# Performance work log

Measured on AMD Instinct MI355X. Metric: run time of the kernel, lower is better.

The kernel has to match this reference:

```python
import jax, jax.numpy as jnp
import numpy as np

B, S, D = 4, 4096, 1024
DC = 1024  # d_chunk (defaults to d_model)
NUM_CLASSES = 4


def setup_inputs() -> dict:
    key = jax.random.key(0)
    ks = jax.random.split(key, 8)
    init = lambda k, shape: (jax.random.normal(k, shape, jnp.float32) * 0.02)
    return {
        "h": jax.random.normal(ks[0], (B, S, D), jnp.float32),
        "pseudo_labels": jax.random.randint(ks[1], (B, S), 0, NUM_CLASSES, jnp.int32),
        "Wl": init(ks[2], (D, NUM_CLASSES)), "bl": jnp.zeros((NUM_CLASSES,), jnp.float32),
        "Wq": init(ks[3], (D, DC)), "bq": jnp.zeros((DC,), jnp.float32),
        "Wk": init(ks[4], (D, DC)), "bk": jnp.zeros((DC,), jnp.float32),
        "Wv": init(ks[5], (D, D)), "bv": jnp.zeros((D,), jnp.float32),
        "Wo": init(ks[6], (D, D)), "bo": jnp.zeros((D,), jnp.float32),
    }


def _chunk_starts(labels):
    """BIOS chunking: label 0=B starts a chunk extended by following 1=I's;
    labels 1 (orphan I), 2=O, 3=S are singleton chunks. Returns bool [B,S]
    marking chunk starts. Parallel replacement for the torch while-loop."""
    def step(ext, lab):  # ext[b]: previous token can be extended by an I
        cont = (lab == 1) & ext          # this token continues prev chunk
        new_ext = (lab == 0) | cont      # B, or a continuing I, is extendable
        return new_ext, ~cont            # non-continuing token starts a chunk
    init = jnp.zeros(labels.shape[0], dtype=bool)
    _, starts_t = jax.lax.scan(step, init, labels.T)  # scan over seq axis
    return starts_t.T  # [B, S]


def reference(h, pseudo_labels, Wl, bl, Wq, bq, Wk, bk, Wv, bv, Wo, bo):
    b, s, d = h.shape
    dc = Wq.shape[1]

    logits = h @ Wl + bl                                  # [B,S,4]
    logp = jax.nn.log_softmax(logits, axis=-1)
    loss = -jnp.mean(jnp.take_along_axis(logp, pseudo_labels[..., None], axis=-1))

    pred = jnp.argmax(logits, axis=-1).astype(jnp.int32)  # [B,S]
    starts = _chunk_starts(pred)
    seg = jnp.cumsum(starts.astype(jnp.int32), axis=1) - 1  # segment id per token

    # Segment-mean pooling, padded to S possible chunks per batch element.
    seg_sum = jax.vmap(lambda x, ids: jax.ops.segment_sum(x, ids, num_segments=s))(h, seg)
    counts = jax.vmap(lambda ids: jax.ops.segment_sum(jnp.ones((s,), h.dtype), ids, num_segments=s))(seg)
    chunk_emb = seg_sum / jnp.maximum(counts, 1.0)[..., None]  # [B,S,D]
    valid = counts > 0                                         # [B,S]

    q = h @ Wq + bq              # [B,S,DC]
    k = chunk_emb @ Wk + bk      # [B,C,DC]
    v = chunk_emb @ Wv + bv      # [B,C,D]
    scale = jnp.asarray(1.0 / np.sqrt(dc), h.dtype)
    scores = jnp.einsum('bsd,bcd->bsc', q, k) * scale
    scores = jnp.where(valid[:, None, :], scores, jnp.asarray(-1e30, h.dtype))
    attn = jax.nn.softmax(scores, axis=-1)
    attended = jnp.einsum('bsc,bcd->bsd', attn, v)
    ch_out = attended @ Wo + bo
    return ch_out, loss
```

## Files before the change

### kernel.cpp

```cpp
#include <hip/hip_runtime.h>

typedef unsigned short u16;
typedef __attribute__((ext_vector_type(8))) short short8;
typedef __attribute__((ext_vector_type(8))) unsigned short ushort8;
typedef __attribute__((ext_vector_type(4))) unsigned short ushort4v;
typedef __attribute__((ext_vector_type(4))) float f32x4;

#define NB 4
#define SS 4096
#define DD 1024
#define CFENCE asm volatile("" ::: "memory")

__device__ __forceinline__ u16 f2bf(float x) {
  unsigned u = __builtin_bit_cast(unsigned, x);
  u = (u + 0x7FFFu + ((u >> 16) & 1u)) >> 16;
  return (u16)u;
}
__device__ __forceinline__ float bf2f(u16 b) {
  unsigned u = ((unsigned)b) << 16;
  return __builtin_bit_cast(float, u);
}
__device__ __forceinline__ void gload16(const void* g, void* l) {
  __builtin_amdgcn_global_load_lds((const __attribute__((address_space(1))) void*)g,
                                   (__attribute__((address_space(3))) void*)l, 16, 0, 0);
}
__device__ __forceinline__ int xcd_swz(int bid, int nwg) {
  const int x = bid & 7, idx = bid >> 3;
  const int q = nwg >> 3, r = nwg & 7;
  return (x < r ? x * (q + 1) : r * (q + 1) + (x - r) * q) + idx;
}

__global__ __launch_bounds__(256) void k_logits(
    const float* __restrict__ h, const int* __restrict__ lab,
    const float* __restrict__ Wl, const float* __restrict__ bl,
    u16* __restrict__ h16, int* __restrict__ pred, float* __restrict__ lossPart)
{
  const int t = threadIdx.x, w = t >> 6, lane = t & 63;
  const int tok = blockIdx.x * 4 + w;
  const float4* h4p = (const float4*)(h + (size_t)tok * DD);
  const float4* wl4 = (const float4*)Wl;
  float p0 = 0.f, p1 = 0.f, p2 = 0.f, p3 = 0.f;
#pragma unroll
  for (int i = 0; i < 4; ++i) {
    const int d = i * 256 + lane * 4;
    float4 hv = h4p[i * 64 + lane];
    ushort4v hb;
    hb[0] = f2bf(hv.x); hb[1] = f2bf(hv.y); hb[2] = f2bf(hv.z); hb[3] = f2bf(hv.w);
    *(ushort4v*)(h16 + (size_t)tok * DD + d) = hb;
    float4 w0 = wl4[d], w1 = wl4[d + 1], w2 = wl4[d + 2], w3 = wl4[d + 3];
    p0 += hv.x * w0.x + hv.y * w1.x + hv.z * w2.x + hv.w * w3.x;
    p1 += hv.x * w0.y + hv.y * w1.y + hv.z * w2.y + hv.w * w3.y;
    p2 += hv.x * w0.z + hv.y * w1.z + hv.z * w2.z + hv.w * w3.z;
    p3 += hv.x * w0.w + hv.y * w1.w + hv.z * w2.w + hv.w * w3.w;
  }
#pragma unroll
  for (int m = 32; m; m >>= 1) {
    p0 += __shfl_xor(p0, m); p1 += __shfl_xor(p1, m);
    p2 += __shfl_xor(p2, m); p3 += __shfl_xor(p3, m);
  }
  __shared__ float ls[4];
  if (lane == 0) {
    float l[4] = {p0 + bl[0], p1 + bl[1], p2 + bl[2], p3 + bl[3]};
    int bi = 0; float bv = l[0];
#pragma unroll
    for (int c = 1; c < 4; ++c) if (l[c] > bv) { bv = l[c]; bi = c; }
    pred[tok] = bi;
    float se = 0.f;
#pragma unroll
    for (int c = 0; c < 4; ++c) se += expf(l[c] - bv);
    float lse = bv + logf(se);
    ls[w] = lse - l[lab[tok]];
  }
  __syncthreads();
  if (t == 0) lossPart[blockIdx.x] = ls[0] + ls[1] + ls[2] + ls[3];
}

__global__ __launch_bounds__(256) void k_wconv(
    const float* __restrict__ W0, const float* __restrict__ W1,
    const float* __restrict__ W2, const float* __restrict__ W3,
    u16* __restrict__ Wt)
{
  const int gid = blockIdx.x * 256 + threadIdx.x;
  const int mat = gid >> 20;
  const int rem = gid & ((1 << 20) - 1);
  const int n = rem >> 10, k = rem & 1023;
  const float* W = (mat == 0) ? W0 : (mat == 1) ? W1 : (mat == 2) ? W2 : W3;
  Wt[((size_t)mat << 20) + (size_t)n * 1024 + k] = f2bf(W[(size_t)k * 1024 + n]);
}

__global__ __launch_bounds__(256) void k_scan(
    const int* __restrict__ pred, int* __restrict__ cstart, int* __restrict__ ccnt)
{
  const int b = blockIdx.x, t = threadIdx.x;
  const int4* p4 = (const int4*)(pred + (size_t)b * SS);
  int labv[16];
#pragma unroll
  for (int i = 0; i < 4; ++i) {
    int4 v = p4[t * 4 + i];
    labv[i * 4 + 0] = v.x; labv[i * 4 + 1] = v.y;
    labv[i * 4 + 2] = v.z; labv[i * 4 + 3] = v.w;
  }
  int A = 0, Bc = 1;
#pragma unroll
  for (int e = 0; e < 16; ++e) {
    int a = (labv[e] == 0), bb = (labv[e] == 1);
    A = a | (bb & A);
    Bc = bb & Bc;
  }
  __shared__ int sA[256], sB[256], sC[256];
  sA[t] = A; sB[t] = Bc;
  __syncthreads();
  for (int off = 1; off < 256; off <<= 1) {
    int pa = 0, pb = 1;
    if (t >= off) { pa = sA[t - off]; pb = sB[t - off]; }
    __syncthreads();
    A = A | (Bc & pa); Bc = Bc & pb;
    sA[t] = A; sB[t] = Bc;
    __syncthreads();
  }
  const int extIn = (t == 0) ? 0 : sA[t - 1];
  int ext = extIn, nst = 0;
#pragma unroll
  for (int e = 0; e < 16; ++e) {
    int cont = (labv[e] == 1) & ext;
    nst += !cont;
    ext = (labv[e] == 0) | cont;
  }
  sC[t] = nst;
  __syncthreads();
  int tot = nst;
  for (int off = 1; off < 256; off <<= 1) {
    int pc = 0;
    if (t >= off) pc = sC[t - off];
    __syncthreads();
    tot += pc;
    sC[t] = tot;
    __syncthreads();
  }
  const int base = tot - nst;
  const int total = sC[255];
  if (t == 0) { ccnt[b] = total; cstart[b * (SS + 1) + total] = SS; }
  ext = extIn; int id = base;
#pragma unroll
  for (int e = 0; e < 16; ++e) {
    int cont = (labv[e] == 1) & ext;
    if (!cont) cstart[b * (SS + 1) + id++] = t * 16 + e;
    ext = (labv[e] == 0) | cont;
  }
}

__global__ __launch_bounds__(256) void k_pool(
    const float* __restrict__ h, const int* __restrict__ cstart,
    const int* __restrict__ ccnt, u16* __restrict__ cemb)
{
  const int t = threadIdx.x, w = t >> 6, lane = t & 63;
  const int gw = blockIdx.x * 4 + w;
  const int b = gw >> 12, c = gw & (SS - 1);
  u16* out = cemb + (size_t)gw * DD + lane * 16;
  if (c >= ccnt[b]) {
    ushort8 z = {0, 0, 0, 0, 0, 0, 0, 0};
    *(ushort8*)out = z; *(ushort8*)(out + 8) = z;
    return;
  }
  const int s0 = cstart[b * (SS + 1) + c], s1 = cstart[b * (SS + 1) + c + 1];
  float acc[16] = {};
  for (int s = s0; s < s1; ++s) {
    const float4* hp = (const float4*)(h + ((size_t)b * SS + s) * DD + lane * 16);
#pragma unroll
    for (int ii = 0; ii < 4; ++ii) {
      float4 v = hp[ii];
      acc[ii * 4 + 0] += v.x; acc[ii * 4 + 1] += v.y;
      acc[ii * 4 + 2] += v.z; acc[ii * 4 + 3] += v.w;
    }
  }
  const float inv = 1.f / (float)(s1 - s0);
  ushort8 o0, o1;
#pragma unroll
  for (int e = 0; e < 8; ++e) { o0[e] = f2bf(acc[e] * inv); o1[e] = f2bf(acc[8 + e] * inv); }
  *(ushort8*)out = o0; *(ushort8*)(out + 8) = o1;
}

template <int OUTF32>
__global__ __launch_bounds__(512, 2) void gemm256(
    const u16* __restrict__ A0p, const u16* __restrict__ A1p,
    const u16* __restrict__ A2p, const u16* __restrict__ A3p,
    const u16* __restrict__ Bt, long strideB,
    void* __restrict__ C0, void* __restrict__ C1,
    void* __restrict__ C2, void* __restrict__ C3,
    const float* __restrict__ bias, float scale, int M, int N, int K)
{
  __shared__ u16 lds[65536];
  u16* ldsA = lds;
  u16* ldsB = lds + 32768;
  const int t = threadIdx.x, lane = t & 63, w = t >> 6;
  const int wr = w >> 2, wc = w & 3;
  const int z = blockIdx.z;
  const u16* A = (z == 0) ? A0p : (z == 1) ? A1p : (z == 2) ? A2p : A3p;
  void* Cp    = (z == 0) ? C0 : (z == 1) ? C1 : (z == 2) ? C2 : C3;
  const u16* B = Bt + (size_t)z * strideB;
  const int bid = blockIdx.y * gridDim.x + blockIdx.x;
  const int swz = xcd_swz(bid, gridDim.x * gridDim.y);
  const int m0 = (swz / gridDim.x) * 256, n0 = (swz % gridDim.x) * 256;

  f32x4 acc[8][4];
#pragma unroll
  for (int i = 0; i < 8; ++i)
#pragma unroll
    for (int j = 0; j < 4; ++j) acc[i][j] = (f32x4){0.f, 0.f, 0.f, 0.f};

  const int trow = t >> 3;
  const u16* Ag = A + (size_t)(m0 + trow) * K + ((t & 7) ^ (trow & 7)) * 8;
  const u16* Bg = B + (size_t)(n0 + trow) * K + ((t & 7) ^ (trow & 7)) * 8;
  u16* dA = ldsA + t * 8;
  u16* dB = ldsB + t * 8;

#define STG_AH0(BUF, KT) { gload16(Ag + (size_t)(KT),            dA + (BUF) * 16384 + 0 * 4096); \
                           gload16(Ag + (size_t)128 * K + (KT),  dA + (BUF) * 16384 + 2 * 4096); }
#define STG_AH1(BUF, KT) { gload16(Ag + (size_t)64 * K + (KT),   dA + (BUF) * 16384 + 1 * 4096); \
                           gload16(Ag + (size_t)192 * K + (KT),  dA + (BUF) * 16384 + 3 * 4096); }
#define STG_B(BUF, KT)   { gload16(Bg + (size_t)(KT),            dB + (BUF) * 16384 + 0 * 4096); \
                           gload16(Bg + (size_t)64 * K + (KT),   dB + (BUF) * 16384 + 1 * 4096); \
                           gload16(Bg + (size_t)128 * K + (KT),  dB + (BUF) * 16384 + 2 * 4096); \
                           gload16(Bg + (size_t)192 * K + (KT),  dB + (BUF) * 16384 + 3 * 4096); }
#define RD_A(BASE, ROFF) \
  { _Pragma("unroll") for (int mi = 0; mi < 4; ++mi) { \
      af[mi][0] = *(const short8*)((BASE) + (wr * 128 + (ROFF) + mi * 16 + lrow) * 64 + co0); \
      af[mi][1] = *(const short8*)((BASE) + (wr * 128 + (ROFF) + mi * 16 + lrow) * 64 + co1); } }
#define RD_B(BASE) \
  { _Pragma("unroll") for (int ni = 0; ni < 4; ++ni) { \
      bf[ni][0] = *(const short8*)((BASE) + (wc * 64 + ni * 16 + lrow) * 64 + co0); \
      bf[ni][1] = *(const short8*)((BASE) + (wc * 64 + ni * 16 + lrow) * 64 + co1); } }
#define MFMA32(MH) \
  { _Pragma("unroll") for (int ks = 0; ks < 2; ++ks) \
    _Pragma("unroll") for (int mi = 0; mi < 4; ++mi) \
      _Pragma("unroll") for (int ni = 0; ni < 4; ++ni) \
        acc[(MH) * 4 + mi][ni] = __builtin_amdgcn_mfma_f32_16x16x32_bf16( \
            af[mi][ks], bf[ni][ks], acc[(MH) * 4 + mi][ni], 0, 0, 0); }

  const int lrow = lane & 15, hi = lane >> 4;
  const int co0 = (hi ^ (lrow & 7)) * 8;
  const int co1 = ((4 + hi) ^ (lrow & 7)) * 8;

  const int NT = K >> 6;
  STG_AH0(0, 0); STG_AH1(0, 0); STG_B(0, 0);
  if (NT > 1) {
    STG_AH0(1, 64); STG_B(1, 64);
    asm volatile("s_waitcnt vmcnt(6)" ::: "memory");
  } else {
    asm volatile("s_waitcnt vmcnt(0)" ::: "memory");
  }
  __builtin_amdgcn_s_barrier();
  CFENCE;

  short8 af[4][2], bf[4][2];
  for (int j = 0; j < NT; ++j) {
    const int cur = j & 1;
    const u16* bufA = ldsA + cur * 16384;
    const u16* bufB = ldsB + cur * 16384;
    RD_A(bufA, 0);
    RD_B(bufB);
    if (j + 1 < NT) STG_AH1(cur ^ 1, (j + 1) << 6);
    CFENCE;
    __builtin_amdgcn_s_barrier();
    __builtin_amdgcn_s_setprio(1);
    MFMA32(0);
    __builtin_amdgcn_s_setprio(0);
    __builtin_amdgcn_sched_barrier(0);
    __builtin_amdgcn_s_barrier();
    CFENCE;
    RD_A(bufA, 64);
    if (j + 2 < NT) { STG_AH0(cur, (j + 2) << 6); STG_B(cur, (j + 2) << 6); }
    CFENCE;
    __builtin_amdgcn_s_barrier();
    __builtin_amdgcn_s_setprio(1);
    MFMA32(1);
    __builtin_amdgcn_s_setprio(0);
    if (j + 2 < NT)       asm volatile("s_waitcnt vmcnt(6)" ::: "memory");
    else if (j + 2 == NT) asm volatile("s_waitcnt vmcnt(0)" ::: "memory");
    __builtin_amdgcn_sched_barrier(0);
    __builtin_amdgcn_s_barrier();
    CFENCE;
  }

  if (OUTF32) {
    const int rowb = m0 + wr * 128 + (lane >> 4) * 4;
#pragma unroll
    for (int n = 0; n < 4; ++n) {
      const int col = n0 + wc * 64 + n * 16 + (lane & 15);
      const float bv = bias ? bias[col] : 0.f;
#pragma unroll
      for (int m = 0; m < 8; ++m)
#pragma unroll
        for (int q = 0; q < 4; ++q)
          ((float*)Cp)[(size_t)(rowb + m * 16 + q) * N + col] = acc[m][n][q] * scale + bv;
    }
  } else {
    __syncthreads();
    u16* cls = lds;
    const int rowl = wr * 128 + (lane >> 4) * 4;
#pragma unroll
    for (int n = 0; n < 4; ++n) {
      const int coll = wc * 64 + n * 16 + (lane & 15);
      const float bv = bias ? bias[n0 + coll] : 0.f;
#pragma unroll
      for (int m = 0; m < 8; ++m)
#pragma unroll
        for (int q = 0; q < 4; ++q)
          cls[(rowl + m * 16 + q) * 256 + coll] = f2bf(acc[m][n][q] * scale + bv);
    }
    __syncthreads();
    u16* Cu = (u16*)Cp;
#pragma unroll
    for (int ps = 0; ps < 16; ++ps) {
      const int f = ps * 512 + t;
      const int row = f >> 5, col8 = (f & 31) * 8;
      *(ushort8*)(Cu + (size_t)(m0 + row) * N + n0 + col8) =
          *(const ushort8*)(cls + row * 256 + col8);
    }
  }
#undef STG_AH0
#undef STG_AH1
#undef STG_B
#undef RD_A
#undef RD_B
#undef MFMA32
}

__global__ __launch_bounds__(256) void k_softmax(
    u16* __restrict__ s0, u16* __restrict__ s1,
    u16* __restrict__ s2, u16* __restrict__ s3, const int* __restrict__ ccnt)
{
  const int t = threadIdx.x, lane = t & 63, w = t >> 6;
  const int row = blockIdx.x, b = blockIdx.y;
  u16* sc = (b == 0) ? s0 : (b == 1) ? s1 : (b == 2) ? s2 : s3;
  const int Cb = ccnt[b];
  u16* p = sc + (size_t)row * SS + t * 16;
  ushort8 v0 = *(ushort8*)p, v1 = *(ushort8*)(p + 8);
  float x[16];
#pragma unroll
  for (int e = 0; e < 8; ++e) { x[e] = bf2f(v0[e]); x[8 + e] = bf2f(v1[e]); }
  const int cb0 = t * 16;
  float m = -1e30f;
#pragma unroll
  for (int e = 0; e < 16; ++e) if (cb0 + e < Cb) m = fmaxf(m, x[e]);
#pragma unroll
  for (int off = 32; off; off >>= 1) m = fmaxf(m, __shfl_xor(m, off));
  __shared__ float red[4], red2[4];
  if (lane == 0) red[w] = m;
  __syncthreads();
  m = fmaxf(fmaxf(red[0], red[1]), fmaxf(red[2], red[3]));
  float ssum = 0.f;
#pragma unroll
  for (int e = 0; e < 16; ++e) {
    float ev = (cb0 + e < Cb) ? __expf(x[e] - m) : 0.f;
    x[e] = ev; ssum += ev;
  }
#pragma unroll
  for (int off = 32; off; off >>= 1) ssum += __shfl_xor(ssum, off);
  if (lane == 0) red2[w] = ssum;
  __syncthreads();
  ssum = red2[0] + red2[1] + red2[2] + red2[3];
  const float inv = 1.f / ssum;
#pragma unroll
  for (int e = 0; e < 8; ++e) { v0[e] = f2bf(x[e] * inv); v1[e] = f2bf(x[8 + e] * inv); }
  *(ushort8*)p = v0; *(ushort8*)(p + 8) = v1;
}

__global__ __launch_bounds__(256) void k_transpose(
    const u16* __restrict__ v, u16* __restrict__ vt)
{
  __shared__ u16 ts[64][80];
  const int t = threadIdx.x;
  const int d0 = blockIdx.x * 64, c0 = blockIdx.y * 64, b = blockIdx.z;
#pragma unroll
  for (int p = 0; p < 2; ++p) {
    const int idx = p * 256 + t, r = idx >> 3, cc = idx & 7;
    ushort8 val = *(const ushort8*)(v + ((size_t)b * SS + c0 + r) * DD + d0 + cc * 8);
    *(ushort8*)&ts[r][cc * 8] = val;
  }
  __syncthreads();
#pragma unroll
  for (int p = 0; p < 2; ++p) {
    const int idx = p * 256 + t, r = idx >> 3, cc = idx & 7;
    ushort8 o;
#pragma unroll
    for (int e = 0; e < 8; ++e) o[e] = ts[cc * 8 + e][r];
    *(ushort8*)(vt + ((size_t)b * DD + d0 + r) * SS + c0 + cc * 8) = o;
  }
}

__global__ __launch_bounds__(256) void k_lossfin(
    const float* __restrict__ part, float* __restrict__ out)
{
  const int t = threadIdx.x, lane = t & 63, w = t >> 6;
  float s = 0.f;
  for (int i = t; i < 4096; i += 256) s += part[i];
#pragma unroll
  for (int off = 32; off; off >>= 1) s += __shfl_xor(s, off);
  __shared__ float r[4];
  if (lane == 0) r[w] = s;
  __syncthreads();
  if (t == 0) out[0] = (r[0] + r[1] + r[2] + r[3]) * (1.f / (NB * SS));
}

extern "C" void kernel_launch(void* const* d_in, const int* in_sizes, int n_in,
                              void* d_out, int out_size, void* d_ws, size_t ws_size,
                              hipStream_t stream) {
  const float* h  = (const float*)d_in[0];
  const int* plab = (const int*)d_in[1];
  const float* Wl = (const float*)d_in[2];
  const float* bl = (const float*)d_in[3];
  const float* Wq = (const float*)d_in[4];
  const float* bq = (const float*)d_in[5];
  const float* Wk = (const float*)d_in[6];
  const float* bk = (const float*)d_in[7];
  const float* Wv = (const float*)d_in[8];
  const float* bv = (const float*)d_in[9];
  const float* Wo = (const float*)d_in[10];
  const float* bo = (const float*)d_in[11];
  float* out = (float*)d_out;

  char* ws = (char*)d_ws;
  const size_t SZ = (size_t)NB * SS * DD * 2;
  const size_t SD = (size_t)SS * DD;
  u16* h16      = (u16*)(ws + 0 * SZ);
  u16* cemb     = (u16*)(ws + 1 * SZ);
  u16* q        = (u16*)(ws + 2 * SZ);
  u16* kk       = (u16*)(ws + 3 * SZ);
  u16* vv       = (u16*)(ws + 4 * SZ);
  u16* vt       = (u16*)(ws + 5 * SZ);
  u16* Wt       = (u16*)(ws + 6 * SZ);
  char* ws2     = ws + 6 * SZ + (size_t)4 * 1024 * 1024 * 2;
  int* pred     = (int*)ws2;
  int* cstart   = (int*)(ws2 + 65536);
  int* ccnt     = (int*)(ws2 + 65536 + 4 * (SS + 1) * 4);
  float* lossPart = (float*)(ws2 + 65536 + 4 * (SS + 1) * 4 + 64);
  u16* s0 = (u16*)d_out;
  u16* s1 = (u16*)d_out + (size_t)SS * SS;
  u16* s2 = h16;
  u16* s3 = cemb;
  u16* att = vv;

  k_logits<<<dim3(NB * SS / 4), 256, 0, stream>>>(h, plab, Wl, bl, h16, pred, lossPart);
  k_wconv<<<dim3(4 * 1024 * 1024 / 256), 256, 0, stream>>>(Wq, Wk, Wv, Wo, Wt);
  k_scan<<<dim3(NB), 256, 0, stream>>>(pred, cstart, ccnt);
  k_pool<<<dim3(NB * SS / 4), 256, 0, stream>>>(h, cstart, ccnt, cemb);

  gemm256<0><<<dim3(DD / 256, NB * SS / 256, 1), 512, 0, stream>>>(
      h16, h16, h16, h16, Wt, 0, q, q, q, q, bq, 1.f, NB * SS, DD, DD);
  gemm256<0><<<dim3(DD / 256, NB * SS / 256, 1), 512, 0, stream>>>(
      cemb, cemb, cemb, cemb, Wt + (1 << 20), 0, kk, kk, kk, kk, bk, 1.f, NB * SS, DD, DD);
  gemm256<0><<<dim3(DD / 256, NB * SS / 256, 1), 512, 0, stream>>>(
      cemb, cemb, cemb, cemb, Wt + 2 * (1 << 20), 0, vv, vv, vv, vv, bv, 1.f, NB * SS, DD, DD);
  k_transpose<<<dim3(DD / 64, SS / 64, NB), 256, 0, stream>>>(vv, vt);

  const float scl = 1.f / 32.f;
  gemm256<0><<<dim3(SS / 256, SS / 256, NB), 512, 0, stream>>>(
      q, q + SD, q + 2 * SD, q + 3 * SD, kk, (long)SD,
      s0, s1, s2, s3, nullptr, scl, SS, SS, DD);
  k_softmax<<<dim3(SS, NB), 256, 0, stream>>>(s0, s1, s2, s3, ccnt);
  gemm256<0><<<dim3(DD / 256, SS / 256, NB), 512, 0, stream>>>(
      s0, s1, s2, s3, vt, (long)SD,
      att, att + SD, att + 2 * SD, att + 3 * SD, nullptr, 1.f, SS, DD, SS);
  gemm256<1><<<dim3(DD / 256, NB * SS / 256, 1), 512, 0, stream>>>(
      att, att, att, att, Wt + 3 * (1 << 20), 0, out, out, out, out, bo, 1.f, NB * SS, DD, DD);
  k_lossfin<<<dim3(1), 256, 0, stream>>>(lossPart, out + (size_t)NB * SS * DD);
}
```

Measured before the change: 550.9 us.

## Fold Wo into Wv, skip invalid chunk columns, clamp PV K-loop

Precomputes Wv·Wo as one fused weight and bv·Wo+bo as a bias, so the final output projection GEMM goes away and the attention-times-V GEMM writes fp32 output directly. The QK^T GEMM skips column tiles beyond the per-batch chunk count, and the PV GEMM clamps its K loop to that count, so work on padded chunks is avoided. Score buffers are moved into reused workspace, which means splitting batch 3's scores across q and kk, and the QK launch is split in two to handle this. The costs are extra small kernels (weight product, bias vector), an additional rounding step from the bf16 fused weight, and data-dependent skipping whose benefit varies with the chunk counts.

```diff
diff --git a/kernel.cpp b/kernel.cpp
--- a/kernel.cpp
+++ b/kernel.cpp
@@ -85,7 +85,8 @@
   const int rem = gid & ((1 << 20) - 1);
   const int n = rem >> 10, k = rem & 1023;
   const float* W = (mat == 0) ? W0 : (mat == 1) ? W1 : (mat == 2) ? W2 : W3;
-  Wt[((size_t)mat << 20) + (size_t)n * 1024 + k] = f2bf(W[(size_t)k * 1024 + n]);
+  const float v = (mat == 2) ? W[(size_t)n * 1024 + k] : W[(size_t)k * 1024 + n];
+  Wt[(size_t)gid] = f2bf(v);
 }
 
 __global__ __launch_bounds__(256) void k_scan(
@@ -180,28 +181,94 @@
   *(ushort8*)out = o0; *(ushort8*)(out + 8) = o1;
 }
 
-template <int OUTF32>
+__global__ __launch_bounds__(256) void k_bvwo(
+    const float* __restrict__ bv, const float* __restrict__ Wo,
+    const float* __restrict__ bo, float* __restrict__ outv)
+{
+  const int n = blockIdx.x * 256 + threadIdx.x;
+  float s = 0.f;
+#pragma unroll 8
+  for (int j = 0; j < 1024; ++j) s += bv[j] * Wo[(size_t)j * 1024 + n];
+  outv[n] = s;
+}
+
+__global__ __launch_bounds__(256) void k_wvo(
+    const u16* __restrict__ WoT, const u16* __restrict__ Wvn, u16* __restrict__ WvoT)
+{
+  __shared__ u16 lA[64 * 64], lB[64 * 64];
+  const int t = threadIdx.x, lane = t & 63, w = t >> 6;
+  const int m0 = blockIdx.y * 64, n0 = blockIdx.x * 64;
+  const int trow = t >> 3;
+  const int schunk = ((t & 7) ^ (trow & 7)) * 8;
+  const u16* Ag = WoT + (size_t)(m0 + trow) * 1024 + schunk;
+  const u16* Bg = Wvn + (size_t)(n0 + trow) * 1024 + schunk;
+  u16* dA = lA + t * 8;
+  u16* dB = lB + t * 8;
+  f32x4 acc[4];
+#pragma unroll
+  for (int i = 0; i < 4; ++i) acc[i] = (f32x4){0.f, 0.f, 0.f, 0.f};
+  const int lrow = lane & 15, hi = lane >> 4;
+  const int co0 = (hi ^ (lrow & 7)) * 8;
+  const int co1 = ((4 + hi) ^ (lrow & 7)) * 8;
+  for (int kt = 0; kt < 1024; kt += 64) {
+    gload16(Ag + kt, dA); gload16(Ag + (size_t)32 * 1024 + kt, dA + 2048);
+    gload16(Bg + kt, dB); gload16(Bg + (size_t)32 * 1024 + kt, dB + 2048);
+    __syncthreads();
+#pragma unroll
+    for (int ks = 0; ks < 2; ++ks) {
+      const int co = ks ? co1 : co0;
+      short8 af = *(const short8*)(lA + (w * 16 + lrow) * 64 + co);
+#pragma unroll
+      for (int ni = 0; ni < 4; ++ni) {
+        short8 bf8 = *(const short8*)(lB + (ni * 16 + lrow) * 64 + co);
+        acc[ni] = __builtin_amdgcn_mfma_f32_16x16x32_bf16(af, bf8, acc[ni], 0, 0, 0);
+      }
+    }
+    __syncthreads();
+  }
+#pragma unroll
+  for (int ni = 0; ni < 4; ++ni)
+#pragma unroll
+    for (int q = 0; q < 4; ++q)
+      WvoT[(size_t)(m0 + w * 16 + hi * 4 + q) * 1024 + n0 + ni * 16 + lrow] = f2bf(acc[ni][q]);
+}
+
+template <int OUTF32, int CLAMPK, int SKIPN>
 __global__ __launch_bounds__(512, 2) void gemm256(
     const u16* __restrict__ A0p, const u16* __restrict__ A1p,
     const u16* __restrict__ A2p, const u16* __restrict__ A3p,
+    const u16* __restrict__ A3bp,
     const u16* __restrict__ Bt, long strideB,
     void* __restrict__ C0, void* __restrict__ C1,
-    void* __restrict__ C2, void* __restrict__ C3,
-    const float* __restrict__ bias, float scale, int M, int N, int K)
+    void* __restrict__ C2, void* __restrict__ C3, void* __restrict__ C3b,
+    const float* __restrict__ bias, float scale, int M, int N, int K,
+    const int* __restrict__ ccnt, int zoff)
 {
   __shared__ u16 lds[65536];
   u16* ldsA = lds;
   u16* ldsB = lds + 32768;
   const int t = threadIdx.x, lane = t & 63, w = t >> 6;
   const int wr = w >> 2, wc = w & 3;
-  const int z = blockIdx.z;
-  const u16* A = (z == 0) ? A0p : (z == 1) ? A1p : (z == 2) ? A2p : A3p;
-  void* Cp    = (z == 0) ? C0 : (z == 1) ? C1 : (z == 2) ? C2 : C3;
-  const u16* B = Bt + (size_t)z * strideB;
+  const int z = blockIdx.z + zoff;
   const int bid = blockIdx.y * gridDim.x + blockIdx.x;
   const int swz = xcd_swz(bid, gridDim.x * gridDim.y);
   const int m0 = (swz / gridDim.x) * 256, n0 = (swz % gridDim.x) * 256;
 
+  int NT = K >> 6;
+  if (SKIPN || CLAMPK) {
+    const int cb = ccnt[z];
+    const int ntc = (cb + 63) >> 6;
+    if (SKIPN && n0 >= (ntc << 6)) return;
+    if (CLAMPK && ntc < NT) NT = ntc;
+  }
+
+  const u16* A = (z == 0) ? A0p : (z == 1) ? A1p : (z == 2) ? A2p : A3p;
+  void* Cp    = (z == 0) ? C0 : (z == 1) ? C1 : (z == 2) ? C2 : C3;
+  int meffA = m0, meffC = m0;
+  if (z == 3 && A3bp && m0 >= 2048) { A = A3bp; meffA = m0 - 2048; }
+  if (z == 3 && C3b && m0 >= 2048) { Cp = C3b; meffC = m0 - 2048; }
+  const u16* B = Bt + (size_t)z * strideB;
+
   f32x4 acc[8][4];
 #pragma unroll
   for (int i = 0; i < 8; ++i)
@@ -209,7 +276,7 @@
     for (int j = 0; j < 4; ++j) acc[i][j] = (f32x4){0.f, 0.f, 0.f, 0.f};
 
   const int trow = t >> 3;
-  const u16* Ag = A + (size_t)(m0 + trow) * K + ((t & 7) ^ (trow & 7)) * 8;
+  const u16* Ag = A + (size_t)(meffA + trow) * K + ((t & 7) ^ (trow & 7)) * 8;
   const u16* Bg = B + (size_t)(n0 + trow) * K + ((t & 7) ^ (trow & 7)) * 8;
   u16* dA = ldsA + t * 8;
   u16* dB = ldsB + t * 8;
@@ -241,7 +308,6 @@
   const int co0 = (hi ^ (lrow & 7)) * 8;
   const int co1 = ((4 + hi) ^ (lrow & 7)) * 8;
 
-  const int NT = K >> 6;
   STG_AH0(0, 0); STG_AH1(0, 0); STG_B(0, 0);
   if (NT > 1) {
     STG_AH0(1, 64); STG_B(1, 64);
@@ -314,7 +380,7 @@
     for (int ps = 0; ps < 16; ++ps) {
       const int f = ps * 512 + t;
       const int row = f >> 5, col8 = (f & 31) * 8;
-      *(ushort8*)(Cu + (size_t)(m0 + row) * N + n0 + col8) =
+      *(ushort8*)(Cu + (size_t)(meffC + row) * N + n0 + col8) =
           *(const ushort8*)(cls + row * 256 + col8);
     }
   }
@@ -327,14 +393,18 @@
 }
 
 __global__ __launch_bounds__(256) void k_softmax(
-    u16* __restrict__ s0, u16* __restrict__ s1,
-    u16* __restrict__ s2, u16* __restrict__ s3, const int* __restrict__ ccnt)
+    u16* __restrict__ s0, u16* __restrict__ s1, u16* __restrict__ s2,
+    u16* __restrict__ s3a, u16* __restrict__ s3b, const int* __restrict__ ccnt)
 {
   const int t = threadIdx.x, lane = t & 63, w = t >> 6;
   const int row = blockIdx.x, b = blockIdx.y;
-  u16* sc = (b == 0) ? s0 : (b == 1) ? s1 : (b == 2) ? s2 : s3;
+  u16* sc;
+  if (b == 0) sc = s0 + (size_t)row * SS;
+  else if (b == 1) sc = s1 + (size_t)row * SS;
+  else if (b == 2) sc = s2 + (size_t)row * SS;
+  else sc = (row < 2048) ? s3a + (size_t)row * SS : s3b + (size_t)(row - 2048) * SS;
   const int Cb = ccnt[b];
-  u16* p = sc + (size_t)row * SS + t * 16;
+  u16* p = sc + t * 16;
   ushort8 v0 = *(ushort8*)p, v1 = *(ushort8*)(p + 8);
   float x[16];
 #pragma unroll
@@ -435,34 +505,42 @@
   int* cstart   = (int*)(ws2 + 65536);
   int* ccnt     = (int*)(ws2 + 65536 + 4 * (SS + 1) * 4);
   float* lossPart = (float*)(ws2 + 65536 + 4 * (SS + 1) * 4 + 64);
-  u16* s0 = (u16*)d_out;
-  u16* s1 = (u16*)d_out + (size_t)SS * SS;
-  u16* s2 = h16;
-  u16* s3 = cemb;
-  u16* att = vv;
+  float* bvwo   = (float*)(ws2 + 65536 + 4 * (SS + 1) * 4 + 64 + 16384);
+  u16* s0 = h16;
+  u16* s1 = cemb;
+  u16* s2 = vv;
+  u16* s3a = q;
+  u16* s3b = kk;
 
   k_logits<<<dim3(NB * SS / 4), 256, 0, stream>>>(h, plab, Wl, bl, h16, pred, lossPart);
   k_wconv<<<dim3(4 * 1024 * 1024 / 256), 256, 0, stream>>>(Wq, Wk, Wv, Wo, Wt);
   k_scan<<<dim3(NB), 256, 0, stream>>>(pred, cstart, ccnt);
   k_pool<<<dim3(NB * SS / 4), 256, 0, stream>>>(h, cstart, ccnt, cemb);
-
-  gemm256<0><<<dim3(DD / 256, NB * SS / 256, 1), 512, 0, stream>>>(
-      h16, h16, h16, h16, Wt, 0, q, q, q, q, bq, 1.f, NB * SS, DD, DD);
-  gemm256<0><<<dim3(DD / 256, NB * SS / 256, 1), 512, 0, stream>>>(
-      cemb, cemb, cemb, cemb, Wt + (1 << 20), 0, kk, kk, kk, kk, bk, 1.f, NB * SS, DD, DD);
-  gemm256<0><<<dim3(DD / 256, NB * SS / 256, 1), 512, 0, stream>>>(
-      cemb, cemb, cemb, cemb, Wt + 2 * (1 << 20), 0, vv, vv, vv, vv, bv, 1.f, NB * SS, DD, DD);
+  k_bvwo<<<dim3(4), 256, 0, stream>>>(bv, Wo, bo, bvwo);
+
+  gemm256<0, 0, 0><<<dim3(DD / 256, NB * SS / 256, 1), 512, 0, stream>>>(
+      h16, h16, h16, h16, nullptr, Wt, 0, q, q, q, q, nullptr,
+      bq, 1.f, NB * SS, DD, DD, nullptr, 0);
+  k_wvo<<<dim3(16, 16), 256, 0, stream>>>(Wt + 3 * (1 << 20), Wt + 2 * (1 << 20), Wt);
+  gemm256<0, 0, 0><<<dim3(DD / 256, NB * SS / 256, 1), 512, 0, stream>>>(
+      cemb, cemb, cemb, cemb, nullptr, Wt + (1 << 20), 0, kk, kk, kk, kk, nullptr,
+      bk, 1.f, NB * SS, DD, DD, nullptr, 0);
+  gemm256<0, 0, 0><<<dim3(DD / 256, NB * SS / 256, 1), 512, 0, stream>>>(
+      cemb, cemb, cemb, cemb, nullptr, Wt, 0, vv, vv, vv, vv, nullptr,
+      bvwo, 1.f, NB * SS, DD, DD, nullptr, 0);
   k_transpose<<<dim3(DD / 64, SS / 64, NB), 256, 0, stream>>>(vv, vt);
 
   const float scl = 1.f / 32.f;
-  gemm256<0><<<dim3(SS / 256, SS / 256, NB), 512, 0, stream>>>(
-      q, q + SD, q + 2 * SD, q + 3 * SD, kk, (long)SD,
-      s0, s1, s2, s3, nullptr, scl, SS, SS, DD);
-  k_softmax<<<dim3(SS, NB), 256, 0, stream>>>(s0, s1, s2, s3, ccnt);
-  gemm256<0><<<dim3(DD / 256, SS / 256, NB), 512, 0, stream>>>(
-      s0, s1, s2, s3, vt, (long)SD,
-      att, att + SD, att + 2 * SD, att + 3 * SD, nullptr, 1.f, SS, DD, SS);
-  gemm256<1><<<dim3(DD / 256, NB * SS / 256, 1), 512, 0, stream>>>(
-      att, att, att, att, Wt + 3 * (1 << 20), 0, out, out, out, out, bo, 1.f, NB * SS, DD, DD);
+  gemm256<0, 0, 1><<<dim3(SS / 256, SS / 256, 3), 512, 0, stream>>>(
+      q, q + SD, q + 2 * SD, nullptr, nullptr, kk, (long)SD,
+      s0, s1, s2, nullptr, nullptr, nullptr, scl, SS, SS, DD, ccnt, 0);
+  gemm256<0, 0, 1><<<dim3(SS / 256, SS / 256, 1), 512, 0, stream>>>(
+      q, q, q, q + 3 * SD, nullptr, kk, (long)SD,
+      nullptr, nullptr, nullptr, s3a, s3b, nullptr, scl, SS, SS, DD, ccnt, 3);
+  k_softmax<<<dim3(SS, NB), 256, 0, stream>>>(s0, s1, s2, s3a, s3b, ccnt);
+  gemm256<1, 1, 0><<<dim3(DD / 256, SS / 256, NB), 512, 0, stream>>>(
+      s0, s1, s2, s3a, s3b, vt, (long)SD,
+      out, out + SD, out + 2 * SD, out + 3 * SD, nullptr,
+      bo, 1.f, SS, DD, SS, ccnt, 0);
   k_lossfin<<<dim3(1), 256, 0, stream>>>(lossPart, out + (size_t)NB * SS * DD);
 }
```

Measured after the change: 559.0 us. No clear change (+1.5%).
